# Performance work log

Hardware: AMD Instinct MI355X
Metric: run time of the kernel (lower is better)

## Reference

```python
import jax, jax.numpy as jnp
import numpy as np

B, S, D, H, HD = 2, 4096, 1024, 16, 64   # batch, seq, hidden, heads, head_dim
BLOCK, W = 64, 8                          # block size, local window in blocks (512 tokens)
ROPE_BASE = 10000.0


def _rope_tables(seq_len, dim, dtype):
    inv_freq = 1.0 / (ROPE_BASE ** (jnp.arange(0, dim, 2, dtype=jnp.float32) / dim))
    t = jnp.arange(seq_len, dtype=jnp.float32)
    freqs = jnp.einsum('i,j->ij', t, inv_freq)          # [S, dim/2]
    emb = jnp.concatenate([freqs, freqs], axis=-1)       # [S, dim]
    return jnp.cos(emb).astype(dtype), jnp.sin(emb).astype(dtype)


def _rotate_half(x):
    x1, x2 = x[..., : x.shape[-1] // 2], x[..., x.shape[-1] // 2:]
    return jnp.concatenate([-x2, x1], axis=-1)


def _apply_rope(q, k, position_ids):
    # q, k: [B, H, S, HD]; position_ids: [B, S]
    cos_t, sin_t = _rope_tables(S, HD, q.dtype)
    cos = cos_t[position_ids][:, None, :, :]             # [B, 1, S, HD]
    sin = sin_t[position_ids][:, None, :, :]
    q_emb = q * cos + _rotate_half(q) * sin
    k_emb = k * cos + _rotate_half(k) * sin
    return q_emb, k_emb


def _block_sparse_attention(q, k, v):
    # Causal block-sparse (sliding window of W blocks), DeepSpeed-style layout.
    # q, k, v: [B, H, S, HD]
    nb = S // BLOCK
    scale = 1.0 / jnp.sqrt(jnp.asarray(HD, q.dtype))
    qb = q.reshape(B, H, nb, BLOCK, HD)
    kb = k.reshape(B, H, nb, BLOCK, HD)
    vb = v.reshape(B, H, nb, BLOCK, HD)
    # block-column indices attended by each block-row: i-W+1 .. i
    idx = jnp.arange(nb)[:, None] - jnp.arange(W - 1, -1, -1)[None, :]   # [nb, W]
    valid = idx >= 0
    idxc = jnp.clip(idx, 0, nb - 1)
    kg = kb[:, :, idxc]                                   # [B, H, nb, W, BLOCK, HD]
    vg = vb[:, :, idxc]
    scores = jnp.einsum('bhnqd,bhnwkd->bhnqwk', qb, kg) * scale  # [B,H,nb,BLOCK,W,BLOCK]
    # absolute positions for causal mask within the window
    qpos = (jnp.arange(nb) * BLOCK)[:, None, None, None] + jnp.arange(BLOCK)[None, :, None, None]  # [nb,BLOCK,1,1]
    kpos = (idxc * BLOCK)[:, None, :, None] + jnp.arange(BLOCK)[None, None, None, :]               # [nb,1,W,BLOCK]
    mask = (kpos <= qpos) & valid[:, None, :, None]       # [nb, BLOCK, W, BLOCK]
    neg = jnp.asarray(-1e9, scores.dtype)
    scores = jnp.where(mask[None, None], scores, neg)
    scores = scores.reshape(B, H, nb, BLOCK, W * BLOCK)
    probs = jax.nn.softmax(scores, axis=-1)
    out = jnp.einsum('bhnqk,bhnkd->bhnqd', probs, vg.reshape(B, H, nb, W * BLOCK, HD))
    return out.reshape(B, H, S, HD)


def setup_inputs() -> dict:
    key = jax.random.key(0)
    ks = jax.random.split(key, 5)
    hidden_states = jax.random.normal(ks[0], (B, S, D), dtype=jnp.float32)
    position_ids = jnp.tile(jnp.arange(S, dtype=jnp.int32)[None, :], (B, 1))
    w_init = lambda k: (jax.random.normal(k, (D, D), dtype=jnp.float32) * 0.02)
    return {
        'hidden_states': hidden_states,
        'position_ids': position_ids,
        'wq': w_init(ks[1]),  # stored [in, out]
        'wk': w_init(ks[2]),
        'wv': w_init(ks[3]),
        'wo': w_init(ks[4]),
    }


def reference(hidden_states, position_ids, wq, wk, wv, wo):
    q = jnp.einsum('bsd,de->bse', hidden_states, wq).reshape(B, S, H, HD).transpose(0, 2, 1, 3)
    k = jnp.einsum('bsd,de->bse', hidden_states, wk).reshape(B, S, H, HD).transpose(0, 2, 1, 3)
    v = jnp.einsum('bsd,de->bse', hidden_states, wv).reshape(B, S, H, HD).transpose(0, 2, 1, 3)
    q, k = _apply_rope(q, k, position_ids)
    attn = _block_sparse_attention(q, k, v)               # [B, H, S, HD]
    attn = attn.transpose(0, 2, 1, 3).reshape(B, S, D)
    return jnp.einsum('bsd,de->bse', attn, wo)
```

## Files before the change

kernel.cpp:

```cpp
#include <hip/hip_runtime.h>
#include <cstdint>
#include <cstddef>

#define B_ 2
#define S_ 4096
#define D_ 1024
#define H_ 16
#define HD_ 64
#define NB_ 64
#define W_ 8
#define M_ (B_*S_)

#define QSCALE 0.18033688011112042f
#define LOG2_10000_OVER_32 0.41524101186092034f

typedef __bf16 bf16_t;
typedef __bf16 bf16x8 __attribute__((ext_vector_type(8)));
typedef float f32x4 __attribute__((ext_vector_type(4)));

#define GLOAD_LDS16(gp, lp) \
  __builtin_amdgcn_global_load_lds((__attribute__((address_space(1))) void*)(gp), \
                                   (__attribute__((address_space(3))) void*)(lp), 16, 0, 0)

__global__ void cast_bf16_kernel(const float* __restrict__ x, bf16_t* __restrict__ y, int n4) {
  int i = blockIdx.x * 256 + threadIdx.x;
  if (i >= n4) return;
  float4 v = ((const float4*)x)[i];
  union { bf16_t b[4]; uint2 u; } cv;
  cv.b[0] = (bf16_t)v.x; cv.b[1] = (bf16_t)v.y; cv.b[2] = (bf16_t)v.z; cv.b[3] = (bf16_t)v.w;
  ((uint2*)y)[i] = cv.u;
}

__global__ void transpose_cast_kernel(const float* __restrict__ w0, const float* __restrict__ w1,
                                      const float* __restrict__ w2, const float* __restrict__ w3,
                                      bf16_t* __restrict__ out) {
  const float* w = (blockIdx.z == 0) ? w0 : (blockIdx.z == 1) ? w1 : (blockIdx.z == 2) ? w2 : w3;
  bf16_t* wt = out + (size_t)blockIdx.z * D_ * D_;
  __shared__ float tile[32][33];
  int x = blockIdx.x * 32 + threadIdx.x;
  int y0 = blockIdx.y * 32;
  for (int i = threadIdx.y; i < 32; i += 8)
    tile[i][threadIdx.x] = w[(size_t)(y0 + i) * D_ + x];
  __syncthreads();
  int x2 = blockIdx.y * 32 + threadIdx.x;
  int y2 = blockIdx.x * 32;
  for (int i = threadIdx.y; i < 32; i += 8)
    wt[(size_t)(y2 + i) * D_ + x2] = (bf16_t)tile[threadIdx.x][i];
}

template<bool OBF>
__global__ __launch_bounds__(256) void gemm128(const bf16_t* __restrict__ A,
                                               const bf16_t* __restrict__ BtBase,
                                               void* __restrict__ Cbase,
                                               const int* __restrict__ pos_ids) {
  const bf16_t* Bt = BtBase + (size_t)blockIdx.z * D_ * D_;
  const int mb = blockIdx.y * 128, nb = blockIdx.x * 128;
  const int tid = threadIdx.x;
  const int wid = tid >> 6, lane = tid & 63;
  const int quad = lane >> 4, l16 = lane & 15;
  const int wr = wid >> 1, wc = wid & 1;

  __shared__ bf16_t As[128 * 32];
  __shared__ bf16_t Bs[128 * 32];

  f32x4 acc[4][4];
#pragma unroll
  for (int mi = 0; mi < 4; ++mi)
#pragma unroll
    for (int ni = 0; ni < 4; ++ni)
      acc[mi][ni] = (f32x4){0.f, 0.f, 0.f, 0.f};

  const int acol = (lane & 3) * 8;
  const int arow0 = wid * 32 + (lane >> 2);
  const bf16_t* gA = A + (size_t)(mb + arow0) * D_ + acol;
  const bf16_t* gB = Bt + (size_t)(nb + arow0) * D_ + acol;

  for (int kt = 0; kt < 32; ++kt) {
    const int k0 = kt * 32;
    __syncthreads();
#pragma unroll
    for (int c = 0; c < 2; ++c) {
      GLOAD_LDS16(gA + (size_t)c * 16 * D_ + k0, As + (wid * 2 + c) * 512);
      GLOAD_LDS16(gB + (size_t)c * 16 * D_ + k0, Bs + (wid * 2 + c) * 512);
    }
    __syncthreads();
    bf16x8 af[4], bfr[4];
#pragma unroll
    for (int mi = 0; mi < 4; ++mi)
      af[mi] = *(const bf16x8*)&As[(wr * 64 + mi * 16 + l16) * 32 + quad * 8];
#pragma unroll
    for (int ni = 0; ni < 4; ++ni)
      bfr[ni] = *(const bf16x8*)&Bs[(wc * 64 + ni * 16 + l16) * 32 + quad * 8];
#pragma unroll
    for (int mi = 0; mi < 4; ++mi)
#pragma unroll
      for (int ni = 0; ni < 4; ++ni)
        acc[mi][ni] = __builtin_amdgcn_mfma_f32_16x16x32_bf16(af[mi], bfr[ni], acc[mi][ni], 0, 0, 0);
  }

  if constexpr (OBF) {
    bf16_t* Cp = (bf16_t*)Cbase + (size_t)blockIdx.z * M_ * D_;
    if (blockIdx.z < 2) {
      const float qsc = (blockIdx.z == 0) ? QSCALE : 1.0f;
      float invf[2];
#pragma unroll
      for (int ni = 0; ni < 2; ++ni)
        invf[ni] = __builtin_exp2f(-(float)(ni * 16 + l16) * LOG2_10000_OVER_32);
#pragma unroll
      for (int mi = 0; mi < 4; ++mi)
#pragma unroll
        for (int r = 0; r < 4; ++r) {
          int row = mb + wr * 64 + mi * 16 + quad * 4 + r;
          float fpos = (float)pos_ids[row];
#pragma unroll
          for (int ni = 0; ni < 2; ++ni) {
            float sn, cs;
            __sincosf(fpos * invf[ni], &sn, &cs);
            float x1 = acc[mi][ni][r], x2 = acc[mi][ni + 2][r];
            int col = nb + wc * 64 + ni * 16 + l16;
            Cp[(size_t)row * D_ + col]      = (bf16_t)((x1 * cs - x2 * sn) * qsc);
            Cp[(size_t)row * D_ + col + 32] = (bf16_t)((x2 * cs + x1 * sn) * qsc);
          }
        }
    } else {
#pragma unroll
      for (int mi = 0; mi < 4; ++mi)
#pragma unroll
        for (int ni = 0; ni < 4; ++ni)
#pragma unroll
          for (int r = 0; r < 4; ++r) {
            int row = mb + wr * 64 + mi * 16 + quad * 4 + r;
            int col = nb + wc * 64 + ni * 16 + l16;
            Cp[(size_t)row * D_ + col] = (bf16_t)acc[mi][ni][r];
          }
    }
  } else {
    float* Cp = (float*)Cbase;
#pragma unroll
    for (int mi = 0; mi < 4; ++mi)
#pragma unroll
      for (int ni = 0; ni < 4; ++ni)
#pragma unroll
        for (int r = 0; r < 4; ++r) {
          int row = mb + wr * 64 + mi * 16 + quad * 4 + r;
          int col = nb + wc * 64 + ni * 16 + l16;
          Cp[(size_t)row * D_ + col] = acc[mi][ni][r];
        }
  }
}

__global__ __launch_bounds__(256) void vt_kernel(const bf16_t* __restrict__ v,
                                                 bf16_t* __restrict__ vt) {
  const int kb = blockIdx.x, h = blockIdx.y, b = blockIdx.z;
  const int tid = threadIdx.x;
  __shared__ bf16_t Ls[64 * 72];
#pragma unroll
  for (int it = 0; it < 2; ++it) {
    int idx = it * 256 + tid;
    int r = idx >> 3, c = (idx & 7) * 8;
    *(uint4*)&Ls[r * 72 + c] = *(const uint4*)&v[((size_t)(b * S_ + kb * 64 + r)) * D_ + h * HD_ + c];
  }
  __syncthreads();
#pragma unroll
  for (int it = 0; it < 2; ++it) {
    int idx = it * 256 + tid;
    int d = idx >> 3, a = idx & 7;
    union { bf16_t bv[8]; uint4 u; } pk;
#pragma unroll
    for (int t = 0; t < 8; ++t) {
      int j = (t & 3) * 16 + 2 * a + (t >> 2);
      pk.bv[t] = Ls[j * 72 + d];
    }
    *(uint4*)&vt[((size_t)(b * H_ + h) * HD_ + d) * S_ + kb * 64 + a * 8] = pk.u;
  }
}

__global__ __launch_bounds__(256) void attn_kernel(const bf16_t* __restrict__ q,
                                                   const bf16_t* __restrict__ k,
                                                   const bf16_t* __restrict__ vt,
                                                   bf16_t* __restrict__ o) {
  const int n = blockIdx.x, h = blockIdx.y, b = blockIdx.z;
  const int tid = threadIdx.x;
  const int wid = tid >> 6, lane = tid & 63;
  const int quad = lane >> 4, l16 = lane & 15;

  __shared__ bf16_t Ks[64 * 72];
  __shared__ bf16_t Vs[64 * 72];
  __shared__ bf16_t Ps[4][16 * 72];

  const size_t rowbase = (size_t)(b * S_ + n * 64);
  const size_t hoff = (size_t)h * HD_;
  const size_t vtbase = (size_t)(b * H_ + h) * HD_ * S_;

  const bf16_t* qrow = q + (rowbase + wid * 16 + l16) * D_ + hoff;
  bf16x8 aq0 = *(const bf16x8*)(qrow + quad * 8);
  bf16x8 aq1 = *(const bf16x8*)(qrow + 32 + quad * 8);

  f32x4 o_acc[4];
#pragma unroll
  for (int t = 0; t < 4; ++t) o_acc[t] = (f32x4){0.f, 0.f, 0.f, 0.f};
  float lsum[4] = {0.f, 0.f, 0.f, 0.f};

  const int srow = tid >> 3;
  const int scol = (tid & 7) * 8;

  const int kb0 = (n >= W_ - 1) ? n - (W_ - 1) : 0;
  for (int kb = kb0; kb <= n; ++kb) {
    __syncthreads();
    const size_t krow = (size_t)(b * S_ + kb * 64);
#pragma unroll
    for (int it = 0; it < 2; ++it) {
      int r = it * 32 + srow;
      *(uint4*)&Ks[r * 72 + scol] = *(const uint4*)&k[(krow + r) * D_ + hoff + scol];
      *(uint4*)&Vs[r * 72 + scol] = *(const uint4*)&vt[vtbase + (size_t)r * S_ + kb * 64 + scol];
    }
    __syncthreads();

    f32x4 sacc[4];
#pragma unroll
    for (int t = 0; t < 4; ++t) sacc[t] = (f32x4){0.f, 0.f, 0.f, 0.f};
#pragma unroll
    for (int t = 0; t < 4; ++t) {
      bf16x8 bk0 = *(const bf16x8*)&Ks[(t * 16 + l16) * 72 + quad * 8];
      bf16x8 bk1 = *(const bf16x8*)&Ks[(t * 16 + l16) * 72 + 32 + quad * 8];
      sacc[t] = __builtin_amdgcn_mfma_f32_16x16x32_bf16(aq0, bk0, sacc[t], 0, 0, 0);
      sacc[t] = __builtin_amdgcn_mfma_f32_16x16x32_bf16(aq1, bk1, sacc[t], 0, 0, 0);
    }

    const bool diag = (kb == n);
#pragma unroll
    for (int r = 0; r < 4; ++r) {
      int qpos = wid * 16 + quad * 4 + r;
      union { bf16_t bv[4]; uint2 u; } pk;
      float rs = 0.f;
#pragma unroll
      for (int t = 0; t < 4; ++t) {
        float p = exp2f(sacc[t][r]);
        if (diag && (t * 16 + l16 > qpos)) p = 0.f;
        rs += p;
        pk.bv[t] = (bf16_t)p;
      }
      lsum[r] += rs;
      *(uint2*)&Ps[wid][(quad * 4 + r) * 72 + l16 * 4] = pk.u;
    }

    bf16x8 pa0 = *(const bf16x8*)&Ps[wid][l16 * 72 + quad * 8];
    bf16x8 pa1 = *(const bf16x8*)&Ps[wid][l16 * 72 + 32 + quad * 8];
#pragma unroll
    for (int t = 0; t < 4; ++t) {
      bf16x8 vb0 = *(const bf16x8*)&Vs[(t * 16 + l16) * 72 + quad * 8];
      bf16x8 vb1 = *(const bf16x8*)&Vs[(t * 16 + l16) * 72 + 32 + quad * 8];
      o_acc[t] = __builtin_amdgcn_mfma_f32_16x16x32_bf16(pa0, vb0, o_acc[t], 0, 0, 0);
      o_acc[t] = __builtin_amdgcn_mfma_f32_16x16x32_bf16(pa1, vb1, o_acc[t], 0, 0, 0);
    }
  }

  float inv[4];
#pragma unroll
  for (int r = 0; r < 4; ++r) {
    float s = lsum[r];
#pragma unroll
    for (int off = 1; off < 16; off <<= 1) s += __shfl_xor(s, off);
    inv[r] = 1.f / s;
  }

#pragma unroll
  for (int t = 0; t < 4; ++t)
#pragma unroll
    for (int r = 0; r < 4; ++r) {
      int row = wid * 16 + quad * 4 + r;
      int col = t * 16 + l16;
      o[(rowbase + row) * D_ + hoff + col] = (bf16_t)(o_acc[t][r] * inv[r]);
    }
}

extern "C" void kernel_launch(void* const* d_in, const int* in_sizes, int n_in,
                              void* d_out, int out_size, void* d_ws, size_t ws_size,
                              hipStream_t stream) {
  const float* hs = (const float*)d_in[0];
  const int* pos  = (const int*)d_in[1];
  const float* wq = (const float*)d_in[2];
  const float* wk = (const float*)d_in[3];
  const float* wv = (const float*)d_in[4];
  const float* wo = (const float*)d_in[5];

  bf16_t* ws   = (bf16_t*)d_ws;
  bf16_t* hsb  = ws;
  bf16_t* wT   = hsb + (size_t)M_ * D_;
  bf16_t* qkv  = wT + (size_t)4 * D_ * D_;
  bf16_t* attn = qkv + (size_t)3 * M_ * D_;
  bf16_t* vtg  = hsb;
  bf16_t* qw = qkv;
  bf16_t* kw = qkv + (size_t)M_ * D_;
  bf16_t* vw = qkv + (size_t)2 * M_ * D_;

  cast_bf16_kernel<<<(M_ * D_ / 4 + 255) / 256, 256, 0, stream>>>(hs, hsb, M_ * D_ / 4);
  transpose_cast_kernel<<<dim3(D_ / 32, D_ / 32, 4), dim3(32, 8), 0, stream>>>(wq, wk, wv, wo, wT);
  gemm128<true><<<dim3(D_ / 128, M_ / 128, 3), 256, 0, stream>>>(hsb, wT, (void*)qkv, pos);
  vt_kernel<<<dim3(NB_, H_, B_), 256, 0, stream>>>(vw, vtg);
  attn_kernel<<<dim3(NB_, H_, B_), 256, 0, stream>>>(qw, kw, vtg, attn);
  gemm128<false><<<dim3(D_ / 128, M_ / 128, 1), 256, 0, stream>>>(attn, wT + (size_t)3 * D_ * D_, d_out, pos);
}
```

Baseline: 256.1 us.

## Fuse V transpose into QKV GEMM epilogue and process two query blocks per attention CTA

The V projection epilogue now writes V directly in the transposed per-head layout the attention kernel expects, so the separate vt_kernel launch and its extra round trip through global memory go away. The attention kernel now handles two adjacent query blocks per workgroup and shares each loaded K/V tile between them, which cuts K/V global loads by roughly half. In exchange the grid is halved (1024 workgroups), register pressure rises, and the V epilogue stores become strided 32-byte writes.

```diff
diff --git a/kernel.cpp b/kernel.cpp
--- a/kernel.cpp
+++ b/kernel.cpp
@@ -52,6 +52,7 @@
 __global__ __launch_bounds__(256) void gemm128(const bf16_t* __restrict__ A,
                                                const bf16_t* __restrict__ BtBase,
                                                void* __restrict__ Cbase,
+                                               bf16_t* __restrict__ vt_out,
                                                const int* __restrict__ pos_ids) {
   const bf16_t* Bt = BtBase + (size_t)blockIdx.z * D_ * D_;
   const int mb = blockIdx.y * 128, nb = blockIdx.x * 128;
@@ -99,8 +100,8 @@
   }
 
   if constexpr (OBF) {
-    bf16_t* Cp = (bf16_t*)Cbase + (size_t)blockIdx.z * M_ * D_;
     if (blockIdx.z < 2) {
+      bf16_t* Cp = (bf16_t*)Cbase + (size_t)blockIdx.z * M_ * D_;
       const float qsc = (blockIdx.z == 0) ? QSCALE : 1.0f;
       float invf[2];
 #pragma unroll
@@ -123,16 +124,23 @@
           }
         }
     } else {
-#pragma unroll
-      for (int mi = 0; mi < 4; ++mi)
-#pragma unroll
-        for (int ni = 0; ni < 4; ++ni)
-#pragma unroll
-          for (int r = 0; r < 4; ++r) {
-            int row = mb + wr * 64 + mi * 16 + quad * 4 + r;
-            int col = nb + wc * 64 + ni * 16 + l16;
-            Cp[(size_t)row * D_ + col] = (bf16_t)acc[mi][ni][r];
-          }
+      int g = 2 * blockIdx.y + wr;
+      int bb = g >> 6, sblk = g & 63;
+      int hh = 2 * blockIdx.x + wc;
+      size_t vbase = (size_t)(bb * H_ + hh) * HD_ * S_;
+#pragma unroll
+      for (int ni = 0; ni < 4; ++ni) {
+        int d = ni * 16 + l16;
+        union { bf16_t bv[16]; uint4 u[2]; } pk;
+#pragma unroll
+        for (int r = 0; r < 4; ++r)
+#pragma unroll
+          for (int mi = 0; mi < 4; ++mi)
+            pk.bv[r * 4 + mi] = (bf16_t)acc[mi][ni][r];
+        size_t addr = vbase + (size_t)d * S_ + sblk * 64 + quad * 16;
+        *(uint4*)&vt_out[addr]     = pk.u[0];
+        *(uint4*)&vt_out[addr + 8] = pk.u[1];
+      }
     }
   } else {
     float* Cp = (float*)Cbase;
@@ -149,37 +157,12 @@
   }
 }
 
-__global__ __launch_bounds__(256) void vt_kernel(const bf16_t* __restrict__ v,
-                                                 bf16_t* __restrict__ vt) {
-  const int kb = blockIdx.x, h = blockIdx.y, b = blockIdx.z;
-  const int tid = threadIdx.x;
-  __shared__ bf16_t Ls[64 * 72];
-#pragma unroll
-  for (int it = 0; it < 2; ++it) {
-    int idx = it * 256 + tid;
-    int r = idx >> 3, c = (idx & 7) * 8;
-    *(uint4*)&Ls[r * 72 + c] = *(const uint4*)&v[((size_t)(b * S_ + kb * 64 + r)) * D_ + h * HD_ + c];
-  }
-  __syncthreads();
-#pragma unroll
-  for (int it = 0; it < 2; ++it) {
-    int idx = it * 256 + tid;
-    int d = idx >> 3, a = idx & 7;
-    union { bf16_t bv[8]; uint4 u; } pk;
-#pragma unroll
-    for (int t = 0; t < 8; ++t) {
-      int j = (t & 3) * 16 + 2 * a + (t >> 2);
-      pk.bv[t] = Ls[j * 72 + d];
-    }
-    *(uint4*)&vt[((size_t)(b * H_ + h) * HD_ + d) * S_ + kb * 64 + a * 8] = pk.u;
-  }
-}
-
 __global__ __launch_bounds__(256) void attn_kernel(const bf16_t* __restrict__ q,
                                                    const bf16_t* __restrict__ k,
                                                    const bf16_t* __restrict__ vt,
                                                    bf16_t* __restrict__ o) {
-  const int n = blockIdx.x, h = blockIdx.y, b = blockIdx.z;
+  const int m = blockIdx.x, h = blockIdx.y, b = blockIdx.z;
+  const int n0 = m * 2, n1 = n0 + 1;
   const int tid = threadIdx.x;
   const int wid = tid >> 6, lane = tid & 63;
   const int quad = lane >> 4, l16 = lane & 15;
@@ -188,24 +171,33 @@
   __shared__ bf16_t Vs[64 * 72];
   __shared__ bf16_t Ps[4][16 * 72];
 
-  const size_t rowbase = (size_t)(b * S_ + n * 64);
   const size_t hoff = (size_t)h * HD_;
   const size_t vtbase = (size_t)(b * H_ + h) * HD_ * S_;
-
-  const bf16_t* qrow = q + (rowbase + wid * 16 + l16) * D_ + hoff;
-  bf16x8 aq0 = *(const bf16x8*)(qrow + quad * 8);
-  bf16x8 aq1 = *(const bf16x8*)(qrow + 32 + quad * 8);
-
-  f32x4 o_acc[4];
-#pragma unroll
-  for (int t = 0; t < 4; ++t) o_acc[t] = (f32x4){0.f, 0.f, 0.f, 0.f};
-  float lsum[4] = {0.f, 0.f, 0.f, 0.f};
+  const size_t rowb[2] = {(size_t)(b * S_ + n0 * 64), (size_t)(b * S_ + n1 * 64)};
+
+  bf16x8 aq[2][2];
+#pragma unroll
+  for (int x = 0; x < 2; ++x) {
+    const bf16_t* qr = q + (rowb[x] + wid * 16 + l16) * D_ + hoff;
+    aq[x][0] = *(const bf16x8*)(qr + quad * 8);
+    aq[x][1] = *(const bf16x8*)(qr + 32 + quad * 8);
+  }
+
+  f32x4 o_acc[2][4];
+  float lsum[2][4];
+#pragma unroll
+  for (int x = 0; x < 2; ++x)
+#pragma unroll
+    for (int t = 0; t < 4; ++t) {
+      o_acc[x][t] = (f32x4){0.f, 0.f, 0.f, 0.f};
+      lsum[x][t] = 0.f;
+    }
 
   const int srow = tid >> 3;
   const int scol = (tid & 7) * 8;
 
-  const int kb0 = (n >= W_ - 1) ? n - (W_ - 1) : 0;
-  for (int kb = kb0; kb <= n; ++kb) {
+  const int kb0 = (n0 >= W_ - 1) ? n0 - (W_ - 1) : 0;
+  for (int kb = kb0; kb <= n1; ++kb) {
     __syncthreads();
     const size_t krow = (size_t)(b * S_ + kb * 64);
 #pragma unroll
@@ -216,62 +208,70 @@
     }
     __syncthreads();
 
-    f32x4 sacc[4];
-#pragma unroll
-    for (int t = 0; t < 4; ++t) sacc[t] = (f32x4){0.f, 0.f, 0.f, 0.f};
-#pragma unroll
-    for (int t = 0; t < 4; ++t) {
-      bf16x8 bk0 = *(const bf16x8*)&Ks[(t * 16 + l16) * 72 + quad * 8];
-      bf16x8 bk1 = *(const bf16x8*)&Ks[(t * 16 + l16) * 72 + 32 + quad * 8];
-      sacc[t] = __builtin_amdgcn_mfma_f32_16x16x32_bf16(aq0, bk0, sacc[t], 0, 0, 0);
-      sacc[t] = __builtin_amdgcn_mfma_f32_16x16x32_bf16(aq1, bk1, sacc[t], 0, 0, 0);
-    }
-
-    const bool diag = (kb == n);
+#pragma unroll
+    for (int x = 0; x < 2; ++x) {
+      const int nx = n0 + x;
+      if (x == 0 ? (kb > n0) : (kb < n1 - (W_ - 1))) continue;
+
+      f32x4 sacc[4];
+#pragma unroll
+      for (int t = 0; t < 4; ++t) sacc[t] = (f32x4){0.f, 0.f, 0.f, 0.f};
+#pragma unroll
+      for (int t = 0; t < 4; ++t) {
+        bf16x8 bk0 = *(const bf16x8*)&Ks[(t * 16 + l16) * 72 + quad * 8];
+        bf16x8 bk1 = *(const bf16x8*)&Ks[(t * 16 + l16) * 72 + 32 + quad * 8];
+        sacc[t] = __builtin_amdgcn_mfma_f32_16x16x32_bf16(aq[x][0], bk0, sacc[t], 0, 0, 0);
+        sacc[t] = __builtin_amdgcn_mfma_f32_16x16x32_bf16(aq[x][1], bk1, sacc[t], 0, 0, 0);
+      }
+
+      const bool diag = (kb == nx);
+#pragma unroll
+      for (int r = 0; r < 4; ++r) {
+        int qpos = wid * 16 + quad * 4 + r;
+        union { bf16_t bv[4]; uint2 u; } pk;
+        float rs = 0.f;
+#pragma unroll
+        for (int t = 0; t < 4; ++t) {
+          float p = __builtin_exp2f(sacc[t][r]);
+          if (diag && (t * 16 + l16 > qpos)) p = 0.f;
+          rs += p;
+          pk.bv[t] = (bf16_t)p;
+        }
+        lsum[x][r] += rs;
+        *(uint2*)&Ps[wid][(quad * 4 + r) * 72 + l16 * 4] = pk.u;
+      }
+
+      bf16x8 pa0 = *(const bf16x8*)&Ps[wid][l16 * 72 + quad * 8];
+      bf16x8 pa1 = *(const bf16x8*)&Ps[wid][l16 * 72 + 32 + quad * 8];
+#pragma unroll
+      for (int t = 0; t < 4; ++t) {
+        bf16x8 vb0 = *(const bf16x8*)&Vs[(t * 16 + l16) * 72 + quad * 8];
+        bf16x8 vb1 = *(const bf16x8*)&Vs[(t * 16 + l16) * 72 + 32 + quad * 8];
+        o_acc[x][t] = __builtin_amdgcn_mfma_f32_16x16x32_bf16(pa0, vb0, o_acc[x][t], 0, 0, 0);
+        o_acc[x][t] = __builtin_amdgcn_mfma_f32_16x16x32_bf16(pa1, vb1, o_acc[x][t], 0, 0, 0);
+      }
+    }
+  }
+
+#pragma unroll
+  for (int x = 0; x < 2; ++x) {
+    float inv[4];
 #pragma unroll
     for (int r = 0; r < 4; ++r) {
-      int qpos = wid * 16 + quad * 4 + r;
-      union { bf16_t bv[4]; uint2 u; } pk;
-      float rs = 0.f;
-#pragma unroll
-      for (int t = 0; t < 4; ++t) {
-        float p = exp2f(sacc[t][r]);
-        if (diag && (t * 16 + l16 > qpos)) p = 0.f;
-        rs += p;
-        pk.bv[t] = (bf16_t)p;
-      }
-      lsum[r] += rs;
-      *(uint2*)&Ps[wid][(quad * 4 + r) * 72 + l16 * 4] = pk.u;
-    }
-
-    bf16x8 pa0 = *(const bf16x8*)&Ps[wid][l16 * 72 + quad * 8];
-    bf16x8 pa1 = *(const bf16x8*)&Ps[wid][l16 * 72 + 32 + quad * 8];
-#pragma unroll
-    for (int t = 0; t < 4; ++t) {
-      bf16x8 vb0 = *(const bf16x8*)&Vs[(t * 16 + l16) * 72 + quad * 8];
-      bf16x8 vb1 = *(const bf16x8*)&Vs[(t * 16 + l16) * 72 + 32 + quad * 8];
-      o_acc[t] = __builtin_amdgcn_mfma_f32_16x16x32_bf16(pa0, vb0, o_acc[t], 0, 0, 0);
-      o_acc[t] = __builtin_amdgcn_mfma_f32_16x16x32_bf16(pa1, vb1, o_acc[t], 0, 0, 0);
-    }
-  }
-
-  float inv[4];
-#pragma unroll
-  for (int r = 0; r < 4; ++r) {
-    float s = lsum[r];
-#pragma unroll
-    for (int off = 1; off < 16; off <<= 1) s += __shfl_xor(s, off);
-    inv[r] = 1.f / s;
-  }
-
-#pragma unroll
-  for (int t = 0; t < 4; ++t)
-#pragma unroll
-    for (int r = 0; r < 4; ++r) {
-      int row = wid * 16 + quad * 4 + r;
-      int col = t * 16 + l16;
-      o[(rowbase + row) * D_ + hoff + col] = (bf16_t)(o_acc[t][r] * inv[r]);
-    }
+      float s = lsum[x][r];
+#pragma unroll
+      for (int off = 1; off < 16; off <<= 1) s += __shfl_xor(s, off);
+      inv[r] = 1.f / s;
+    }
+#pragma unroll
+    for (int t = 0; t < 4; ++t)
+#pragma unroll
+      for (int r = 0; r < 4; ++r) {
+        int row = wid * 16 + quad * 4 + r;
+        int col = t * 16 + l16;
+        o[(rowb[x] + row) * D_ + hoff + col] = (bf16_t)(o_acc[x][t][r] * inv[r]);
+      }
+  }
 }
 
 extern "C" void kernel_launch(void* const* d_in, const int* in_sizes, int n_in,
@@ -289,15 +289,13 @@
   bf16_t* wT   = hsb + (size_t)M_ * D_;
   bf16_t* qkv  = wT + (size_t)4 * D_ * D_;
   bf16_t* attn = qkv + (size_t)3 * M_ * D_;
-  bf16_t* vtg  = hsb;
-  bf16_t* qw = qkv;
-  bf16_t* kw = qkv + (size_t)M_ * D_;
-  bf16_t* vw = qkv + (size_t)2 * M_ * D_;
+  bf16_t* qw  = qkv;
+  bf16_t* kw  = qkv + (size_t)M_ * D_;
+  bf16_t* vtg = qkv + (size_t)2 * M_ * D_;
 
   cast_bf16_kernel<<<(M_ * D_ / 4 + 255) / 256, 256, 0, stream>>>(hs, hsb, M_ * D_ / 4);
   transpose_cast_kernel<<<dim3(D_ / 32, D_ / 32, 4), dim3(32, 8), 0, stream>>>(wq, wk, wv, wo, wT);
-  gemm128<true><<<dim3(D_ / 128, M_ / 128, 3), 256, 0, stream>>>(hsb, wT, (void*)qkv, pos);
-  vt_kernel<<<dim3(NB_, H_, B_), 256, 0, stream>>>(vw, vtg);
-  attn_kernel<<<dim3(NB_, H_, B_), 256, 0, stream>>>(qw, kw, vtg, attn);
-  gemm128<false><<<dim3(D_ / 128, M_ / 128, 1), 256, 0, stream>>>(attn, wT + (size_t)3 * D_ * D_, d_out, pos);
-}
+  gemm128<true><<<dim3(D_ / 128, M_ / 128, 3), 256, 0, stream>>>(hsb, wT, (void*)qkv, vtg, pos);
+  attn_kernel<<<dim3(NB_ / 2, H_, B_), 256, 0, stream>>>(qw, kw, vtg, attn);
+  gemm128<false><<<dim3(D_ / 128, M_ / 128, 1), 256, 0, stream>>>(attn, wT + (size_t)3 * D_ * D_, d_out, nullptr, pos);
+}
```

New measurement: 244.8 us. 1.05x faster.
